# Kernel tuning notes

Hardware: AMD Instinct MI355X
Metric: run time of the kernel (lower is better)

Reference implementation:

```python
import jax, jax.numpy as jnp
import numpy as np

N_NODES = 50000
N_EDGES = 500000
F_IN = 128
HIDDEN = 128
N_CLASSES = 32
N_GRAPHS = 64


def setup_inputs() -> dict:
    key = jax.random.key(0)
    ks = jax.random.split(key, 16)
    x = jax.random.normal(ks[0], (N_NODES, F_IN), dtype=jnp.float32)
    edge_index = jax.random.randint(ks[1], (2, N_EDGES), 0, N_NODES, dtype=jnp.int64)
    batch = jnp.sort(jax.random.randint(ks[2], (N_NODES,), 0, N_GRAPHS, dtype=jnp.int64))
    d = {"x": x, "edge_index": edge_index, "batch": batch}
    dims = [(F_IN, HIDDEN)] + [(HIDDEN, HIDDEN)] * 4
    for i, (fi, fo) in enumerate(dims, start=1):
        s = 1.0 / np.sqrt(fi)
        d[f"W{i}"] = jax.random.uniform(ks[2 + i], (fi, fo), jnp.float32, -s, s)
        d[f"b{i}"] = jnp.zeros((fo,), jnp.float32)
    s = 1.0 / np.sqrt(HIDDEN)
    d["W_lin"] = jax.random.uniform(ks[10], (HIDDEN, N_CLASSES), jnp.float32, -s, s)
    d["b_lin"] = jnp.zeros((N_CLASSES,), jnp.float32)
    return d


def _gcn_conv(x, W, b, src, dst, norm_edge, norm_self):
    # PyG GCNConv: h = x @ W; out[dst] += norm * h[src]; + self-loop + bias
    h = x @ W
    msg = h[src] * norm_edge[:, None]                      # [E, F] gather + scale
    agg = jax.ops.segment_sum(msg, dst, num_segments=x.shape[0])  # scatter-add
    return agg + h * norm_self[:, None] + b


def reference(x, edge_index, batch, W1, b1, W2, b2, W3, b3, W4, b4, W5, b5, W_lin, b_lin):
    src, dst = edge_index[0], edge_index[1]
    n = x.shape[0]
    # degree with self-loops (in-degree at dst, +1 for the self loop)
    deg = jax.ops.segment_sum(jnp.ones_like(dst, dtype=x.dtype), dst, num_segments=n) + 1.0
    dis = jax.lax.rsqrt(deg)
    norm_edge = dis[src] * dis[dst]   # per-edge symmetric normalization
    norm_self = dis * dis             # self-loop coefficient = 1/deg

    h = jax.nn.relu(_gcn_conv(x, W1, b1, src, dst, norm_edge, norm_self))
    h = jax.nn.relu(_gcn_conv(h, W2, b2, src, dst, norm_edge, norm_self))
    h = jax.nn.relu(_gcn_conv(h, W3, b3, src, dst, norm_edge, norm_self))
    h = jax.nn.relu(_gcn_conv(h, W4, b4, src, dst, norm_edge, norm_self))
    h = _gcn_conv(h, W5, b5, src, dst, norm_edge, norm_self)

    # global mean pool over graphs in the batch
    sums = jax.ops.segment_sum(h, batch, num_segments=N_GRAPHS)
    counts = jax.ops.segment_sum(jnp.ones((n,), h.dtype), batch, num_segments=N_GRAPHS)
    pooled = sums / jnp.maximum(counts, 1.0)[:, None]
    # dropout is identity in eval mode
    return pooled @ W_lin + b_lin
```

## Files before the change

kernel.cpp:

```cpp
#include <hip/hip_runtime.h>
#include <hip/hip_bf16.h>

#define N_NODES   50000
#define N_EDGES   500000
#define FDIM      128
#define N_CLASSES 32
#define N_GRAPHS  64


__global__ void deg_kernel(const int* __restrict__ dst, int* __restrict__ deg, int E) {
    int e = blockIdx.x * blockDim.x + threadIdx.x;
    if (e < E) atomicAdd(&deg[dst[e]], 1);
}

__global__ void dis_kernel(const int* __restrict__ deg, float* __restrict__ dis, int n) {
    int v = blockIdx.x * blockDim.x + threadIdx.x;
    if (v < n) dis[v] = rsqrtf((float)deg[v] + 1.0f);
}

__global__ void scan_partial(const int* __restrict__ deg, int* __restrict__ part, int n) {
    __shared__ int s[512];
    int t = threadIdx.x;
    int i = blockIdx.x * 512 + t;
    s[t] = (i < n) ? deg[i] : 0;
    __syncthreads();
    for (int o = 256; o > 0; o >>= 1) {
        if (t < o) s[t] += s[t + o];
        __syncthreads();
    }
    if (t == 0) part[blockIdx.x] = s[0];
}

__global__ void scan_offsets(int* part, int nb) {
    if (blockIdx.x == 0 && threadIdx.x == 0) {
        int acc = 0;
        for (int i = 0; i < nb; i++) { int v = part[i]; part[i] = acc; acc += v; }
    }
}

__global__ void scan_final(const int* __restrict__ deg, const int* __restrict__ part,
                           int* __restrict__ rowptr, int n) {
    __shared__ int s[512];
    int t = threadIdx.x;
    int i = blockIdx.x * 512 + t;
    int v = (i < n) ? deg[i] : 0;
    s[t] = v;
    __syncthreads();
    for (int o = 1; o < 512; o <<= 1) {
        int x = (t >= o) ? s[t - o] : 0;
        __syncthreads();
        s[t] += x;
        __syncthreads();
    }
    if (i < n) rowptr[i] = part[blockIdx.x] + s[t] - v;
}

__global__ void fill_csr(const int* __restrict__ src, const int* __restrict__ dst,
                         const int* __restrict__ rowptr, int* __restrict__ fill,
                         const float* __restrict__ dis,
                         int2* __restrict__ csr_sw, int E) {
    int e = blockIdx.x * blockDim.x + threadIdx.x;
    if (e >= E) return;
    int d = dst[e], s = src[e];
    int pos = rowptr[d] + atomicAdd(&fill[d], 1);
    float w = dis[s] * dis[d];
    csr_sw[pos] = make_int2(s, __float_as_int(w));
}


__global__ __launch_bounds__(256) void gemm128(const float* __restrict__ X,
                                               const float* __restrict__ W,
                                               float* __restrict__ H, int n) {
    __shared__ __align__(16) float xs[32][132];
    __shared__ __align__(16) float ws[32][132];
    int t = threadIdx.x;
    int i = t & 15;
    int j = t >> 4;
    int rowBase = blockIdx.x * 128;

    float acc[8][8];
#pragma unroll
    for (int r = 0; r < 8; r++)
#pragma unroll
        for (int c = 0; c < 8; c++) acc[r][c] = 0.f;

    for (int k0 = 0; k0 < 128; k0 += 32) {
        __syncthreads();
        {
            int kq = t & 7, r0 = t >> 3;
#pragma unroll
            for (int p = 0; p < 4; p++) {
                int r = r0 + 32 * p;
                int grow = rowBase + r;
                float4 v = make_float4(0.f, 0.f, 0.f, 0.f);
                if (grow < n) v = *(const float4*)(X + (size_t)grow * FDIM + k0 + kq * 4);
                xs[kq * 4 + 0][r] = v.x;
                xs[kq * 4 + 1][r] = v.y;
                xs[kq * 4 + 2][r] = v.z;
                xs[kq * 4 + 3][r] = v.w;
            }
        }
        {
            int c4 = t & 31, kr = t >> 5;
#pragma unroll
            for (int p = 0; p < 4; p++) {
                int k = kr + 8 * p;
                float4 v = *(const float4*)(W + (size_t)(k0 + k) * FDIM + c4 * 4);
                *(float4*)&ws[k][c4 * 4] = v;
            }
        }
        __syncthreads();
#pragma unroll 8
        for (int k = 0; k < 32; k++) {
            float4 a0 = *(const float4*)&xs[k][i * 4];
            float4 a1 = *(const float4*)&xs[k][i * 4 + 64];
            float4 b0 = *(const float4*)&ws[k][j * 4];
            float4 b1 = *(const float4*)&ws[k][j * 4 + 64];
            float ar[8] = {a0.x, a0.y, a0.z, a0.w, a1.x, a1.y, a1.z, a1.w};
            float br[8] = {b0.x, b0.y, b0.z, b0.w, b1.x, b1.y, b1.z, b1.w};
#pragma unroll
            for (int r = 0; r < 8; r++)
#pragma unroll
                for (int c = 0; c < 8; c++) acc[r][c] = fmaf(ar[r], br[c], acc[r][c]);
        }
    }

#pragma unroll
    for (int rr = 0; rr < 8; rr++) {
        int r = (rr < 4) ? (i * 4 + rr) : (64 + i * 4 + (rr - 4));
        int grow = rowBase + r;
        if (grow < n) {
            float4 o0 = {acc[rr][0], acc[rr][1], acc[rr][2], acc[rr][3]};
            float4 o1 = {acc[rr][4], acc[rr][5], acc[rr][6], acc[rr][7]};
            *(float4*)(H + (size_t)grow * FDIM + j * 4) = o0;
            *(float4*)(H + (size_t)grow * FDIM + j * 4 + 64) = o1;
        }
    }
}


__global__ __launch_bounds__(256) void agg_kernel(const float* __restrict__ H,
                                                  float* __restrict__ OUT,
                                                  const int* __restrict__ rowptr,
                                                  const int* __restrict__ degi,
                                                  const int2* __restrict__ csr_sw,
                                                  const float* __restrict__ dis,
                                                  const float* __restrict__ bias,
                                                  int n, int relu) {
    int wid = (blockIdx.x * blockDim.x + threadIdx.x) >> 6;
    int lane = threadIdx.x & 63;
    if (wid >= n) return;
    int v = wid;
    const int2* sw = csr_sw + rowptr[v];
    int cnt = degi[v];
    float ax = 0.f, ay = 0.f;
    int e = 0;

    for (; e + 8 <= cnt; e += 8) {
        int2 p0 = sw[e + 0], p1 = sw[e + 1], p2 = sw[e + 2], p3 = sw[e + 3];
        int2 p4 = sw[e + 4], p5 = sw[e + 5], p6 = sw[e + 6], p7 = sw[e + 7];
        float2 m0 = *(const float2*)(H + (size_t)p0.x * FDIM + lane * 2);
        float2 m1 = *(const float2*)(H + (size_t)p1.x * FDIM + lane * 2);
        float2 m2 = *(const float2*)(H + (size_t)p2.x * FDIM + lane * 2);
        float2 m3 = *(const float2*)(H + (size_t)p3.x * FDIM + lane * 2);
        float2 m4 = *(const float2*)(H + (size_t)p4.x * FDIM + lane * 2);
        float2 m5 = *(const float2*)(H + (size_t)p5.x * FDIM + lane * 2);
        float2 m6 = *(const float2*)(H + (size_t)p6.x * FDIM + lane * 2);
        float2 m7 = *(const float2*)(H + (size_t)p7.x * FDIM + lane * 2);
        ax = fmaf(__int_as_float(p0.y), m0.x, ax); ay = fmaf(__int_as_float(p0.y), m0.y, ay);
        ax = fmaf(__int_as_float(p1.y), m1.x, ax); ay = fmaf(__int_as_float(p1.y), m1.y, ay);
        ax = fmaf(__int_as_float(p2.y), m2.x, ax); ay = fmaf(__int_as_float(p2.y), m2.y, ay);
        ax = fmaf(__int_as_float(p3.y), m3.x, ax); ay = fmaf(__int_as_float(p3.y), m3.y, ay);
        ax = fmaf(__int_as_float(p4.y), m4.x, ax); ay = fmaf(__int_as_float(p4.y), m4.y, ay);
        ax = fmaf(__int_as_float(p5.y), m5.x, ax); ay = fmaf(__int_as_float(p5.y), m5.y, ay);
        ax = fmaf(__int_as_float(p6.y), m6.x, ax); ay = fmaf(__int_as_float(p6.y), m6.y, ay);
        ax = fmaf(__int_as_float(p7.y), m7.x, ax); ay = fmaf(__int_as_float(p7.y), m7.y, ay);
    }
    for (; e + 4 <= cnt; e += 4) {
        int2 p0 = sw[e + 0], p1 = sw[e + 1], p2 = sw[e + 2], p3 = sw[e + 3];
        float2 m0 = *(const float2*)(H + (size_t)p0.x * FDIM + lane * 2);
        float2 m1 = *(const float2*)(H + (size_t)p1.x * FDIM + lane * 2);
        float2 m2 = *(const float2*)(H + (size_t)p2.x * FDIM + lane * 2);
        float2 m3 = *(const float2*)(H + (size_t)p3.x * FDIM + lane * 2);
        ax = fmaf(__int_as_float(p0.y), m0.x, ax); ay = fmaf(__int_as_float(p0.y), m0.y, ay);
        ax = fmaf(__int_as_float(p1.y), m1.x, ax); ay = fmaf(__int_as_float(p1.y), m1.y, ay);
        ax = fmaf(__int_as_float(p2.y), m2.x, ax); ay = fmaf(__int_as_float(p2.y), m2.y, ay);
        ax = fmaf(__int_as_float(p3.y), m3.x, ax); ay = fmaf(__int_as_float(p3.y), m3.y, ay);
    }
    for (; e < cnt; e++) {
        int2 p = sw[e];
        float2 m = *(const float2*)(H + (size_t)p.x * FDIM + lane * 2);
        ax = fmaf(__int_as_float(p.y), m.x, ax);
        ay = fmaf(__int_as_float(p.y), m.y, ay);
    }

    float dv = dis[v];
    float ns = dv * dv;
    float2 hv = *(const float2*)(H + (size_t)v * FDIM + lane * 2);
    float2 bb = *(const float2*)(bias + lane * 2);
    float ox = ax + ns * hv.x + bb.x;
    float oy = ay + ns * hv.y + bb.y;
    if (relu) { ox = fmaxf(ox, 0.f); oy = fmaxf(oy, 0.f); }
    *(float2*)(OUT + (size_t)v * FDIM + lane * 2) = make_float2(ox, oy);
}


#define POOL_BLOCKS 1024

__global__ __launch_bounds__(128) void pool_kernel(const float* __restrict__ H,
                                                   const int* __restrict__ batch,
                                                   float* __restrict__ psum,
                                                   float* __restrict__ pcnt, int n) {
    int t = threadIdx.x;
    int chunk = (n + POOL_BLOCKS - 1) / POOL_BLOCKS;
    int lo = blockIdx.x * chunk;
    int hi = lo + chunk; if (hi > n) hi = n;
    if (lo >= hi) return;

    float acc = 0.f;
    int cnt = 0;
    int curg = batch[lo];
    float hv = H[(size_t)lo * FDIM + t];
    int g = curg;
    for (int v = lo; v < hi; v++) {
        float hcur = hv;
        int gcur = g;
        if (v + 1 < hi) {
            hv = H[(size_t)(v + 1) * FDIM + t];
            g = batch[v + 1];
        }
        if (gcur != curg) {
            atomicAdd(&psum[curg * FDIM + t], acc);
            if (t == 0) atomicAdd(&pcnt[curg], (float)cnt);
            acc = 0.f; cnt = 0; curg = gcur;
        }
        acc += hcur;
        cnt++;
    }
    atomicAdd(&psum[curg * FDIM + t], acc);
    if (t == 0) atomicAdd(&pcnt[curg], (float)cnt);
}

__global__ void final_lin(const float* __restrict__ psum, const float* __restrict__ pcnt,
                          const float* __restrict__ Wl, const float* __restrict__ bl,
                          float* __restrict__ out) {
    int t = blockIdx.x * blockDim.x + threadIdx.x;
    if (t >= N_GRAPHS * N_CLASSES) return;
    int g = t >> 5, c = t & 31;
    float inv = 1.0f / fmaxf(pcnt[g], 1.0f);
    float s = 0.f;
    for (int k = 0; k < FDIM; k++) s = fmaf(psum[g * FDIM + k], Wl[k * N_CLASSES + c], s);
    out[t] = s * inv + bl[c];
}


static inline size_t align256(size_t x) { return (x + 255) & ~(size_t)255; }

extern "C" void kernel_launch(void* const* d_in, const int* in_sizes, int n_in,
                              void* d_out, int out_size, void* d_ws, size_t ws_size,
                              hipStream_t stream) {
    const float* x     = (const float*)d_in[0];
    const int*   ei    = (const int*)d_in[1];
    const int*   batch = (const int*)d_in[2];
    const float* Wls[5] = {(const float*)d_in[3], (const float*)d_in[5], (const float*)d_in[7],
                           (const float*)d_in[9], (const float*)d_in[11]};
    const float* bls[5] = {(const float*)d_in[4], (const float*)d_in[6], (const float*)d_in[8],
                           (const float*)d_in[10], (const float*)d_in[12]};
    const float* W_lin = (const float*)d_in[13];
    const float* b_lin = (const float*)d_in[14];
    float* out = (float*)d_out;

    const int N = N_NODES, E = N_EDGES;
    const int* src = ei;
    const int* dst = ei + E;

    char* p = (char*)d_ws;
    size_t off = 0;
    float* hA = (float*)(p + off); off = align256(off + (size_t)N * FDIM * 4);
    float* hB = (float*)(p + off); off = align256(off + (size_t)N * FDIM * 4);
    int*   deg = (int*)(p + off); off = align256(off + (size_t)N * 4);
    float* dis = (float*)(p + off); off = align256(off + (size_t)N * 4);
    int*   rowptr = (int*)(p + off); off = align256(off + (size_t)N * 4);
    int*   fill = (int*)(p + off); off = align256(off + (size_t)N * 4);
    int*   part = (int*)(p + off); off = align256(off + 512);
    int2*  csr_sw = (int2*)(p + off); off = align256(off + (size_t)E * 8);
    float* psum = (float*)(p + off); off = align256(off + (size_t)N_GRAPHS * FDIM * 4);
    float* pcnt = (float*)(p + off); off = align256(off + (size_t)N_GRAPHS * 4);
    (void)ws_size; (void)n_in; (void)in_sizes; (void)out_size;

    hipMemsetAsync(deg, 0, (size_t)N * 4, stream);
    hipMemsetAsync(fill, 0, (size_t)N * 4, stream);
    hipMemsetAsync(psum, 0, (size_t)N_GRAPHS * FDIM * 4, stream);
    hipMemsetAsync(pcnt, 0, (size_t)N_GRAPHS * 4, stream);

    deg_kernel<<<(E + 255) / 256, 256, 0, stream>>>(dst, deg, E);
    dis_kernel<<<(N + 255) / 256, 256, 0, stream>>>(deg, dis, N);
    int nChunks = (N + 511) / 512;
    scan_partial<<<nChunks, 512, 0, stream>>>(deg, part, N);
    scan_offsets<<<1, 64, 0, stream>>>(part, nChunks);
    scan_final<<<nChunks, 512, 0, stream>>>(deg, part, rowptr, N);
    fill_csr<<<(E + 255) / 256, 256, 0, stream>>>(src, dst, rowptr, fill, dis,
                                                  csr_sw, E);

    int gemmBlocks = (N + 127) / 128;
    int aggBlocks = (N * 64 + 255) / 256;
    const float* cur = x;
    for (int l = 0; l < 5; l++) {
        gemm128<<<gemmBlocks, 256, 0, stream>>>(cur, Wls[l], hA, N);
        int relu = (l < 4) ? 1 : 0;
        agg_kernel<<<aggBlocks, 256, 0, stream>>>(hA, hB, rowptr, deg, csr_sw,
                                                  dis, bls[l], N, relu);
        cur = hB;
    }

    pool_kernel<<<POOL_BLOCKS, 128, 0, stream>>>(hB, batch, psum, pcnt, N);
    final_lin<<<(N_GRAPHS * N_CLASSES + 255) / 256, 256, 0, stream>>>(psum, pcnt, W_lin,
                                                                      b_lin, out);
}
```

Before: 479.9 us.

## Shrink GEMM row tile to 32 and aggregate two nodes per wavefront

The GEMM now tiles 32 rows per block with a 2x8 register tile instead of 128 rows with 8x8, giving about 1563 blocks rather than 391 so more CUs stay busy. The aggregation kernel assigns two destination nodes to each wavefront and interleaves their edge gathers, which doubles the independent loads in flight per wave. In exchange the GEMM reuses less data from shared memory, since each block reloads the full W tile for fewer rows. Interleaving the two nodes also makes work uneven when their degrees differ, and the code assumes N is even, because the second node v0+1 is not bounds-checked.

New measurement: 498.6 us. +3.9%, slower.

```diff
diff --git a/kernel.cpp b/kernel.cpp
--- a/kernel.cpp
+++ b/kernel.cpp
@@ -68,37 +68,33 @@
 }
 
 
-__global__ __launch_bounds__(256) void gemm128(const float* __restrict__ X,
-                                               const float* __restrict__ W,
-                                               float* __restrict__ H, int n) {
-    __shared__ __align__(16) float xs[32][132];
+__global__ __launch_bounds__(256) void gemm32(const float* __restrict__ X,
+                                              const float* __restrict__ W,
+                                              float* __restrict__ H, int n) {
+    __shared__ __align__(16) float xs[32][36];
     __shared__ __align__(16) float ws[32][132];
     int t = threadIdx.x;
-    int i = t & 15;
-    int j = t >> 4;
-    int rowBase = blockIdx.x * 128;
-
-    float acc[8][8];
-#pragma unroll
-    for (int r = 0; r < 8; r++)
+    int ti = t & 15;
+    int tj = t >> 4;
+    int rowBase = blockIdx.x * 32;
+
+    float acc[2][8];
+#pragma unroll
+    for (int r = 0; r < 2; r++)
 #pragma unroll
         for (int c = 0; c < 8; c++) acc[r][c] = 0.f;
 
     for (int k0 = 0; k0 < 128; k0 += 32) {
         __syncthreads();
         {
-            int kq = t & 7, r0 = t >> 3;
-#pragma unroll
-            for (int p = 0; p < 4; p++) {
-                int r = r0 + 32 * p;
-                int grow = rowBase + r;
-                float4 v = make_float4(0.f, 0.f, 0.f, 0.f);
-                if (grow < n) v = *(const float4*)(X + (size_t)grow * FDIM + k0 + kq * 4);
-                xs[kq * 4 + 0][r] = v.x;
-                xs[kq * 4 + 1][r] = v.y;
-                xs[kq * 4 + 2][r] = v.z;
-                xs[kq * 4 + 3][r] = v.w;
-            }
+            int r = t >> 3, kq = t & 7;
+            int grow = rowBase + r;
+            float4 v = make_float4(0.f, 0.f, 0.f, 0.f);
+            if (grow < n) v = *(const float4*)(X + (size_t)grow * FDIM + k0 + kq * 4);
+            xs[kq * 4 + 0][r] = v.x;
+            xs[kq * 4 + 1][r] = v.y;
+            xs[kq * 4 + 2][r] = v.z;
+            xs[kq * 4 + 3][r] = v.w;
         }
         {
             int c4 = t & 31, kr = t >> 5;
@@ -112,32 +108,63 @@
         __syncthreads();
 #pragma unroll 8
         for (int k = 0; k < 32; k++) {
-            float4 a0 = *(const float4*)&xs[k][i * 4];
-            float4 a1 = *(const float4*)&xs[k][i * 4 + 64];
-            float4 b0 = *(const float4*)&ws[k][j * 4];
-            float4 b1 = *(const float4*)&ws[k][j * 4 + 64];
-            float ar[8] = {a0.x, a0.y, a0.z, a0.w, a1.x, a1.y, a1.z, a1.w};
+            float2 a = *(const float2*)&xs[k][ti * 2];
+            float4 b0 = *(const float4*)&ws[k][tj * 4];
+            float4 b1 = *(const float4*)&ws[k][tj * 4 + 64];
             float br[8] = {b0.x, b0.y, b0.z, b0.w, b1.x, b1.y, b1.z, b1.w};
 #pragma unroll
-            for (int r = 0; r < 8; r++)
-#pragma unroll
-                for (int c = 0; c < 8; c++) acc[r][c] = fmaf(ar[r], br[c], acc[r][c]);
-        }
-    }
-
-#pragma unroll
-    for (int rr = 0; rr < 8; rr++) {
-        int r = (rr < 4) ? (i * 4 + rr) : (64 + i * 4 + (rr - 4));
-        int grow = rowBase + r;
+            for (int c = 0; c < 8; c++) {
+                acc[0][c] = fmaf(a.x, br[c], acc[0][c]);
+                acc[1][c] = fmaf(a.y, br[c], acc[1][c]);
+            }
+        }
+    }
+
+#pragma unroll
+    for (int rr = 0; rr < 2; rr++) {
+        int grow = rowBase + ti * 2 + rr;
         if (grow < n) {
             float4 o0 = {acc[rr][0], acc[rr][1], acc[rr][2], acc[rr][3]};
             float4 o1 = {acc[rr][4], acc[rr][5], acc[rr][6], acc[rr][7]};
-            *(float4*)(H + (size_t)grow * FDIM + j * 4) = o0;
-            *(float4*)(H + (size_t)grow * FDIM + j * 4 + 64) = o1;
-        }
-    }
-}
-
+            *(float4*)(H + (size_t)grow * FDIM + tj * 4) = o0;
+            *(float4*)(H + (size_t)grow * FDIM + tj * 4 + 64) = o1;
+        }
+    }
+}
+
+
+#define GATH4(SW, E0, AX, AY)                                                  \
+    {                                                                          \
+        int2 q0 = SW[E0], q1 = SW[E0 + 1], q2 = SW[E0 + 2], q3 = SW[E0 + 3];   \
+        float2 n0 = *(const float2*)(H + (size_t)q0.x * FDIM + lane * 2);      \
+        float2 n1 = *(const float2*)(H + (size_t)q1.x * FDIM + lane * 2);      \
+        float2 n2 = *(const float2*)(H + (size_t)q2.x * FDIM + lane * 2);      \
+        float2 n3 = *(const float2*)(H + (size_t)q3.x * FDIM + lane * 2);      \
+        AX = fmaf(__int_as_float(q0.y), n0.x, AX);                             \
+        AY = fmaf(__int_as_float(q0.y), n0.y, AY);                             \
+        AX = fmaf(__int_as_float(q1.y), n1.x, AX);                             \
+        AY = fmaf(__int_as_float(q1.y), n1.y, AY);                             \
+        AX = fmaf(__int_as_float(q2.y), n2.x, AX);                             \
+        AY = fmaf(__int_as_float(q2.y), n2.y, AY);                             \
+        AX = fmaf(__int_as_float(q3.y), n3.x, AX);                             \
+        AY = fmaf(__int_as_float(q3.y), n3.y, AY);                             \
+    }
+
+__device__ __forceinline__ void drain_edges(const float* __restrict__ H,
+                                            const int2* __restrict__ sw, int cnt,
+                                            int& e, int lane, float& ax, float& ay) {
+    for (; e + 8 <= cnt; e += 8) {
+        GATH4(sw, e, ax, ay);
+        GATH4(sw, e + 4, ax, ay);
+    }
+    for (; e + 4 <= cnt; e += 4) GATH4(sw, e, ax, ay);
+    for (; e < cnt; e++) {
+        int2 p = sw[e];
+        float2 m = *(const float2*)(H + (size_t)p.x * FDIM + lane * 2);
+        ax = fmaf(__int_as_float(p.y), m.x, ax);
+        ay = fmaf(__int_as_float(p.y), m.y, ay);
+    }
+}
 
 __global__ __launch_bounds__(256) void agg_kernel(const float* __restrict__ H,
                                                   float* __restrict__ OUT,
@@ -149,59 +176,50 @@
                                                   int n, int relu) {
     int wid = (blockIdx.x * blockDim.x + threadIdx.x) >> 6;
     int lane = threadIdx.x & 63;
-    if (wid >= n) return;
-    int v = wid;
-    const int2* sw = csr_sw + rowptr[v];
-    int cnt = degi[v];
-    float ax = 0.f, ay = 0.f;
-    int e = 0;
-
-    for (; e + 8 <= cnt; e += 8) {
-        int2 p0 = sw[e + 0], p1 = sw[e + 1], p2 = sw[e + 2], p3 = sw[e + 3];
-        int2 p4 = sw[e + 4], p5 = sw[e + 5], p6 = sw[e + 6], p7 = sw[e + 7];
-        float2 m0 = *(const float2*)(H + (size_t)p0.x * FDIM + lane * 2);
-        float2 m1 = *(const float2*)(H + (size_t)p1.x * FDIM + lane * 2);
-        float2 m2 = *(const float2*)(H + (size_t)p2.x * FDIM + lane * 2);
-        float2 m3 = *(const float2*)(H + (size_t)p3.x * FDIM + lane * 2);
-        float2 m4 = *(const float2*)(H + (size_t)p4.x * FDIM + lane * 2);
-        float2 m5 = *(const float2*)(H + (size_t)p5.x * FDIM + lane * 2);
-        float2 m6 = *(const float2*)(H + (size_t)p6.x * FDIM + lane * 2);
-        float2 m7 = *(const float2*)(H + (size_t)p7.x * FDIM + lane * 2);
-        ax = fmaf(__int_as_float(p0.y), m0.x, ax); ay = fmaf(__int_as_float(p0.y), m0.y, ay);
-        ax = fmaf(__int_as_float(p1.y), m1.x, ax); ay = fmaf(__int_as_float(p1.y), m1.y, ay);
-        ax = fmaf(__int_as_float(p2.y), m2.x, ax); ay = fmaf(__int_as_float(p2.y), m2.y, ay);
-        ax = fmaf(__int_as_float(p3.y), m3.x, ax); ay = fmaf(__int_as_float(p3.y), m3.y, ay);
-        ax = fmaf(__int_as_float(p4.y), m4.x, ax); ay = fmaf(__int_as_float(p4.y), m4.y, ay);
-        ax = fmaf(__int_as_float(p5.y), m5.x, ax); ay = fmaf(__int_as_float(p5.y), m5.y, ay);
-        ax = fmaf(__int_as_float(p6.y), m6.x, ax); ay = fmaf(__int_as_float(p6.y), m6.y, ay);
-        ax = fmaf(__int_as_float(p7.y), m7.x, ax); ay = fmaf(__int_as_float(p7.y), m7.y, ay);
-    }
-    for (; e + 4 <= cnt; e += 4) {
-        int2 p0 = sw[e + 0], p1 = sw[e + 1], p2 = sw[e + 2], p3 = sw[e + 3];
-        float2 m0 = *(const float2*)(H + (size_t)p0.x * FDIM + lane * 2);
-        float2 m1 = *(const float2*)(H + (size_t)p1.x * FDIM + lane * 2);
-        float2 m2 = *(const float2*)(H + (size_t)p2.x * FDIM + lane * 2);
-        float2 m3 = *(const float2*)(H + (size_t)p3.x * FDIM + lane * 2);
-        ax = fmaf(__int_as_float(p0.y), m0.x, ax); ay = fmaf(__int_as_float(p0.y), m0.y, ay);
-        ax = fmaf(__int_as_float(p1.y), m1.x, ax); ay = fmaf(__int_as_float(p1.y), m1.y, ay);
-        ax = fmaf(__int_as_float(p2.y), m2.x, ax); ay = fmaf(__int_as_float(p2.y), m2.y, ay);
-        ax = fmaf(__int_as_float(p3.y), m3.x, ax); ay = fmaf(__int_as_float(p3.y), m3.y, ay);
-    }
-    for (; e < cnt; e++) {
-        int2 p = sw[e];
-        float2 m = *(const float2*)(H + (size_t)p.x * FDIM + lane * 2);
-        ax = fmaf(__int_as_float(p.y), m.x, ax);
-        ay = fmaf(__int_as_float(p.y), m.y, ay);
-    }
-
-    float dv = dis[v];
-    float ns = dv * dv;
-    float2 hv = *(const float2*)(H + (size_t)v * FDIM + lane * 2);
+    int v0 = wid * 2;
+    if (v0 >= n) return;
+    int v1 = v0 + 1;
+
+    const int2* sw0 = csr_sw + rowptr[v0];
+    const int2* sw1 = csr_sw + rowptr[v1];
+    int c0 = degi[v0], c1 = degi[v1];
+    float a0x = 0.f, a0y = 0.f, a1x = 0.f, a1y = 0.f;
+    int e0 = 0, e1 = 0;
+
+    while (e0 + 8 <= c0 && e1 + 8 <= c1) {
+        GATH4(sw0, e0, a0x, a0y);
+        GATH4(sw0, e0 + 4, a0x, a0y);
+        GATH4(sw1, e1, a1x, a1y);
+        GATH4(sw1, e1 + 4, a1x, a1y);
+        e0 += 8; e1 += 8;
+    }
+    while (e0 + 4 <= c0 && e1 + 4 <= c1) {
+        GATH4(sw0, e0, a0x, a0y);
+        GATH4(sw1, e1, a1x, a1y);
+        e0 += 4; e1 += 4;
+    }
+    drain_edges(H, sw0, c0, e0, lane, a0x, a0y);
+    drain_edges(H, sw1, c1, e1, lane, a1x, a1y);
+
     float2 bb = *(const float2*)(bias + lane * 2);
-    float ox = ax + ns * hv.x + bb.x;
-    float oy = ay + ns * hv.y + bb.y;
-    if (relu) { ox = fmaxf(ox, 0.f); oy = fmaxf(oy, 0.f); }
-    *(float2*)(OUT + (size_t)v * FDIM + lane * 2) = make_float2(ox, oy);
+    {
+        float dv = dis[v0];
+        float ns = dv * dv;
+        float2 hv = *(const float2*)(H + (size_t)v0 * FDIM + lane * 2);
+        float ox = a0x + ns * hv.x + bb.x;
+        float oy = a0y + ns * hv.y + bb.y;
+        if (relu) { ox = fmaxf(ox, 0.f); oy = fmaxf(oy, 0.f); }
+        *(float2*)(OUT + (size_t)v0 * FDIM + lane * 2) = make_float2(ox, oy);
+    }
+    {
+        float dv = dis[v1];
+        float ns = dv * dv;
+        float2 hv = *(const float2*)(H + (size_t)v1 * FDIM + lane * 2);
+        float ox = a1x + ns * hv.x + bb.x;
+        float oy = a1y + ns * hv.y + bb.y;
+        if (relu) { ox = fmaxf(ox, 0.f); oy = fmaxf(oy, 0.f); }
+        *(float2*)(OUT + (size_t)v1 * FDIM + lane * 2) = make_float2(ox, oy);
+    }
 }
 
 
@@ -302,11 +320,11 @@
     fill_csr<<<(E + 255) / 256, 256, 0, stream>>>(src, dst, rowptr, fill, dis,
                                                   csr_sw, E);
 
-    int gemmBlocks = (N + 127) / 128;
-    int aggBlocks = (N * 64 + 255) / 256;
+    int gemmBlocks = (N + 31) / 32;
+    int aggBlocks = ((N / 2) * 64 + 255) / 256;
     const float* cur = x;
     for (int l = 0; l < 5; l++) {
-        gemm128<<<gemmBlocks, 256, 0, stream>>>(cur, Wls[l], hA, N);
+        gemm32<<<gemmBlocks, 256, 0, stream>>>(cur, Wls[l], hA, N);
         int relu = (l < 4) ? 1 : 0;
         agg_kernel<<<aggBlocks, 256, 0, stream>>>(hA, hB, rowptr, deg, csr_sw,
                                                   dis, bls[l], N, relu);
```

## Shrink GEMM tile to 32 rows, fuse dis into scan, merge memsets

Applied to the files above, without the earlier changes.

The 128x128 GEMM tile with 8x8 per-thread accumulators becomes a 32x128 tile with 4x4 accumulators. This launches four times as many blocks (about 1563 instead of 391) and uses fewer registers, so the 256 CUs get more blocks and waves. The dis computation moves into scan_partial, which removes one launch. The workspace is reordered so the four zeroed buffers sit next to each other and one memset clears them all. The cost is lower arithmetic intensity per thread and the W tile being reloaded by four times as many blocks.

After: 448.9 us. 6.5% less time.

```diff
diff --git a/kernel.cpp b/kernel.cpp
--- a/kernel.cpp
+++ b/kernel.cpp
@@ -13,16 +13,14 @@
     if (e < E) atomicAdd(&deg[dst[e]], 1);
 }
 
-__global__ void dis_kernel(const int* __restrict__ deg, float* __restrict__ dis, int n) {
-    int v = blockIdx.x * blockDim.x + threadIdx.x;
-    if (v < n) dis[v] = rsqrtf((float)deg[v] + 1.0f);
-}
-
-__global__ void scan_partial(const int* __restrict__ deg, int* __restrict__ part, int n) {
+__global__ void scan_partial(const int* __restrict__ deg, int* __restrict__ part,
+                             float* __restrict__ dis, int n) {
     __shared__ int s[512];
     int t = threadIdx.x;
     int i = blockIdx.x * 512 + t;
-    s[t] = (i < n) ? deg[i] : 0;
+    int d = (i < n) ? deg[i] : 0;
+    if (i < n) dis[i] = rsqrtf((float)d + 1.0f);
+    s[t] = d;
     __syncthreads();
     for (int o = 256; o > 0; o >>= 1) {
         if (t < o) s[t] += s[t + o];
@@ -68,37 +66,33 @@
 }
 
 
-__global__ __launch_bounds__(256) void gemm128(const float* __restrict__ X,
-                                               const float* __restrict__ W,
-                                               float* __restrict__ H, int n) {
-    __shared__ __align__(16) float xs[32][132];
+__global__ __launch_bounds__(256) void gemm32(const float* __restrict__ X,
+                                              const float* __restrict__ W,
+                                              float* __restrict__ H, int n) {
+    __shared__ __align__(16) float xs[32][36];
     __shared__ __align__(16) float ws[32][132];
     int t = threadIdx.x;
-    int i = t & 15;
-    int j = t >> 4;
-    int rowBase = blockIdx.x * 128;
-
-    float acc[8][8];
-#pragma unroll
-    for (int r = 0; r < 8; r++)
-#pragma unroll
-        for (int c = 0; c < 8; c++) acc[r][c] = 0.f;
+    int ti = t & 7;
+    int tj = t >> 3;
+    int rowBase = blockIdx.x * 32;
+
+    float acc[4][4];
+#pragma unroll
+    for (int r = 0; r < 4; r++)
+#pragma unroll
+        for (int c = 0; c < 4; c++) acc[r][c] = 0.f;
 
     for (int k0 = 0; k0 < 128; k0 += 32) {
         __syncthreads();
         {
-            int kq = t & 7, r0 = t >> 3;
-#pragma unroll
-            for (int p = 0; p < 4; p++) {
-                int r = r0 + 32 * p;
-                int grow = rowBase + r;
-                float4 v = make_float4(0.f, 0.f, 0.f, 0.f);
-                if (grow < n) v = *(const float4*)(X + (size_t)grow * FDIM + k0 + kq * 4);
-                xs[kq * 4 + 0][r] = v.x;
-                xs[kq * 4 + 1][r] = v.y;
-                xs[kq * 4 + 2][r] = v.z;
-                xs[kq * 4 + 3][r] = v.w;
-            }
+            int r = t >> 3, kq = t & 7;
+            int grow = rowBase + r;
+            float4 v = make_float4(0.f, 0.f, 0.f, 0.f);
+            if (grow < n) v = *(const float4*)(X + (size_t)grow * FDIM + k0 + kq * 4);
+            xs[kq * 4 + 0][r] = v.x;
+            xs[kq * 4 + 1][r] = v.y;
+            xs[kq * 4 + 2][r] = v.z;
+            xs[kq * 4 + 3][r] = v.w;
         }
         {
             int c4 = t & 31, kr = t >> 5;
@@ -112,28 +106,23 @@
         __syncthreads();
 #pragma unroll 8
         for (int k = 0; k < 32; k++) {
-            float4 a0 = *(const float4*)&xs[k][i * 4];
-            float4 a1 = *(const float4*)&xs[k][i * 4 + 64];
-            float4 b0 = *(const float4*)&ws[k][j * 4];
-            float4 b1 = *(const float4*)&ws[k][j * 4 + 64];
-            float ar[8] = {a0.x, a0.y, a0.z, a0.w, a1.x, a1.y, a1.z, a1.w};
-            float br[8] = {b0.x, b0.y, b0.z, b0.w, b1.x, b1.y, b1.z, b1.w};
-#pragma unroll
-            for (int r = 0; r < 8; r++)
-#pragma unroll
-                for (int c = 0; c < 8; c++) acc[r][c] = fmaf(ar[r], br[c], acc[r][c]);
-        }
-    }
-
-#pragma unroll
-    for (int rr = 0; rr < 8; rr++) {
-        int r = (rr < 4) ? (i * 4 + rr) : (64 + i * 4 + (rr - 4));
-        int grow = rowBase + r;
+            float4 a = *(const float4*)&xs[k][ti * 4];
+            float4 b = *(const float4*)&ws[k][tj * 4];
+            float ar[4] = {a.x, a.y, a.z, a.w};
+            float br[4] = {b.x, b.y, b.z, b.w};
+#pragma unroll
+            for (int r = 0; r < 4; r++)
+#pragma unroll
+                for (int c = 0; c < 4; c++) acc[r][c] = fmaf(ar[r], br[c], acc[r][c]);
+        }
+    }
+
+#pragma unroll
+    for (int rr = 0; rr < 4; rr++) {
+        int grow = rowBase + ti * 4 + rr;
         if (grow < n) {
-            float4 o0 = {acc[rr][0], acc[rr][1], acc[rr][2], acc[rr][3]};
-            float4 o1 = {acc[rr][4], acc[rr][5], acc[rr][6], acc[rr][7]};
-            *(float4*)(H + (size_t)grow * FDIM + j * 4) = o0;
-            *(float4*)(H + (size_t)grow * FDIM + j * 4 + 64) = o1;
+            float4 o = {acc[rr][0], acc[rr][1], acc[rr][2], acc[rr][3]};
+            *(float4*)(H + (size_t)grow * FDIM + tj * 4) = o;
         }
     }
 }
@@ -278,35 +267,33 @@
     size_t off = 0;
     float* hA = (float*)(p + off); off = align256(off + (size_t)N * FDIM * 4);
     float* hB = (float*)(p + off); off = align256(off + (size_t)N * FDIM * 4);
-    int*   deg = (int*)(p + off); off = align256(off + (size_t)N * 4);
+    int2*  csr_sw = (int2*)(p + off); off = align256(off + (size_t)E * 8);
     float* dis = (float*)(p + off); off = align256(off + (size_t)N * 4);
     int*   rowptr = (int*)(p + off); off = align256(off + (size_t)N * 4);
+    int*   part = (int*)(p + off); off = align256(off + 512);
+    size_t zero_off = off;
+    int*   deg = (int*)(p + off); off = align256(off + (size_t)N * 4);
     int*   fill = (int*)(p + off); off = align256(off + (size_t)N * 4);
-    int*   part = (int*)(p + off); off = align256(off + 512);
-    int2*  csr_sw = (int2*)(p + off); off = align256(off + (size_t)E * 8);
     float* psum = (float*)(p + off); off = align256(off + (size_t)N_GRAPHS * FDIM * 4);
     float* pcnt = (float*)(p + off); off = align256(off + (size_t)N_GRAPHS * 4);
+    size_t zero_bytes = off - zero_off;
     (void)ws_size; (void)n_in; (void)in_sizes; (void)out_size;
 
-    hipMemsetAsync(deg, 0, (size_t)N * 4, stream);
-    hipMemsetAsync(fill, 0, (size_t)N * 4, stream);
-    hipMemsetAsync(psum, 0, (size_t)N_GRAPHS * FDIM * 4, stream);
-    hipMemsetAsync(pcnt, 0, (size_t)N_GRAPHS * 4, stream);
+    hipMemsetAsync(p + zero_off, 0, zero_bytes, stream);
 
     deg_kernel<<<(E + 255) / 256, 256, 0, stream>>>(dst, deg, E);
-    dis_kernel<<<(N + 255) / 256, 256, 0, stream>>>(deg, dis, N);
     int nChunks = (N + 511) / 512;
-    scan_partial<<<nChunks, 512, 0, stream>>>(deg, part, N);
+    scan_partial<<<nChunks, 512, 0, stream>>>(deg, part, dis, N);
     scan_offsets<<<1, 64, 0, stream>>>(part, nChunks);
     scan_final<<<nChunks, 512, 0, stream>>>(deg, part, rowptr, N);
     fill_csr<<<(E + 255) / 256, 256, 0, stream>>>(src, dst, rowptr, fill, dis,
                                                   csr_sw, E);
 
-    int gemmBlocks = (N + 127) / 128;
+    int gemmBlocks = (N + 31) / 32;
     int aggBlocks = (N * 64 + 255) / 256;
     const float* cur = x;
     for (int l = 0; l < 5; l++) {
-        gemm128<<<gemmBlocks, 256, 0, stream>>>(cur, Wls[l], hA, N);
+        gemm32<<<gemmBlocks, 256, 0, stream>>>(cur, Wls[l], hA, N);
         int relu = (l < 4) ? 1 : 0;
         agg_kernel<<<aggBlocks, 256, 0, stream>>>(hA, hB, rowptr, deg, csr_sw,
                                                   dis, bls[l], N, relu);
```
